# Optimization experiments

Measured on AMD Instinct MI355X. Metric: run time of the kernel, lower is better.

## Reference

```python
import jax, jax.numpy as jnp
import numpy as np

B, S, D = 4, 1024, 1024
DB = 128           # d_bottleneck (router embedding dim)
R = 128            # neuron bottleneck rank
N_QK, N_V, N_KNOW = 2048, 2048, 4096
MB_QK, MB_V, MB_KNOW = 16, 16, 32
H = 16
EPS = 1e-8


def _unit(k, shape):
    v = jax.random.normal(k, shape, jnp.float32)
    return v / (jnp.linalg.norm(v, axis=-1, keepdims=True) + EPS)


def setup_inputs() -> dict:
    key = jax.random.key(0)
    ks = jax.random.split(key, 16)
    s = 0.02
    nrm = lambda k, sh, sc=0.02: jax.random.normal(k, sh, jnp.float32) * sc
    return {
        "x": jax.random.normal(ks[0], (B, S, D), jnp.float32),
        "qk_emb": _unit(ks[1], (N_QK, DB)),
        "v_emb": _unit(ks[2], (N_V, DB)),
        "know_emb": _unit(ks[3], (N_KNOW, DB)),
        "qk_f": nrm(ks[4], (MB_QK, D, R)),
        "qk_r": nrm(ks[5], (MB_QK, R, D)),
        "v_f": nrm(ks[6], (MB_V, D, R)),
        "v_r": nrm(ks[7], (MB_V, R, D)),
        "know_f": nrm(ks[8], (MB_KNOW, D, R)),
        "know_r": nrm(ks[9], (MB_KNOW, R, D)),
        "proj_attn_k": nrm(ks[10], (D, 3 * DB)),
        "proj_attn_b": jnp.zeros((3 * DB,), jnp.float32),
        "tau_attn_k": nrm(ks[11], (D, 3)),
        "tau_attn_b": jnp.zeros((3,), jnp.float32),
        "proj_know_k": nrm(ks[12], (D, DB)),
        "proj_know_b": jnp.zeros((DB,), jnp.float32),
        "tau_know_k": nrm(ks[13], (D, 1)),
        "tau_know_b": jnp.zeros((1,), jnp.float32),
        "expand_O": nrm(ks[14], (D, D)),
        "ln1_scale": jnp.ones((D,), jnp.float32),
        "ln1_bias": jnp.zeros((D,), jnp.float32),
        "ln2_scale": jnp.ones((D,), jnp.float32),
        "ln2_bias": jnp.zeros((D,), jnp.float32),
    }


def layer_norm(x, scale, bias, eps=1e-6):
    mean = jnp.mean(x, axis=-1, keepdims=True)
    var = jnp.mean(jnp.square(x - mean), axis=-1, keepdims=True)
    return (x - mean) / jnp.sqrt(var + eps) * scale + bias


def threshold_gate(scores, tau):
    gate = jnp.maximum(scores - tau, 0.0)
    return gate / (gate.sum(axis=-1, keepdims=True) + EPS)


def group_gate(gate, n_basis):
    b, s, n = gate.shape  # n divisible by n_basis here
    g = gate.reshape(b, s, n_basis, n // n_basis).sum(axis=-1)
    return g / (g.sum(axis=-1, keepdims=True) + EPS)


@jax.checkpoint
def feature_fn(x, neurons, weights):
    all_h = jnp.einsum('bsd,ndr->bsnr', x, neurons)
    return jnp.einsum('bsnr,bsn->bsr', all_h, weights)


@jax.checkpoint
def restore_fn(h, neurons, weights):
    pre = jnp.einsum('bsr,bsn->bsnr', h, weights)
    return jnp.einsum('bsnr,nrd->bsd', pre, neurons)


def reference(x, qk_emb, v_emb, know_emb, qk_f, qk_r, v_f, v_r, know_f, know_r,
              proj_attn_k, proj_attn_b, tau_attn_k, tau_attn_b,
              proj_know_k, proj_know_b, tau_know_k, tau_know_b,
              expand_O, ln1_scale, ln1_bias, ln2_scale, ln2_bias):
    # ---- attention circuit (pre-LN) ----
    n1 = layer_norm(x, ln1_scale, ln1_bias)
    qk_n = qk_emb / (jnp.linalg.norm(qk_emb, axis=-1, keepdims=True) + EPS)
    v_n = v_emb / (jnp.linalg.norm(v_emb, axis=-1, keepdims=True) + EPS)
    h_all = n1 @ proj_attn_k + proj_attn_b            # [B,S,3*DB]
    h_q, h_k, h_v = jnp.split(h_all, 3, axis=-1)
    tau = n1 @ tau_attn_k + tau_attn_b                # [B,S,3]
    g_q = threshold_gate(h_q @ qk_n.T, tau[:, :, 0:1])
    g_k = threshold_gate(h_k @ qk_n.T, tau[:, :, 1:2])
    g_v = threshold_gate(h_v @ v_n.T, tau[:, :, 2:3])
    gq_b = group_gate(g_q, MB_QK)
    gk_b = group_gate(g_k, MB_QK)
    gv_b = group_gate(g_v, MB_V)
    Q = restore_fn(feature_fn(n1, qk_f, gq_b), qk_r, gq_b)
    K = restore_fn(feature_fn(n1, qk_f, gk_b), qk_r, gk_b)
    V = restore_fn(feature_fn(n1, v_f, gv_b), v_r, gv_b)
    d_head = D // H
    Q = Q.reshape(B, S, H, d_head).transpose(0, 2, 1, 3)
    K = K.reshape(B, S, H, d_head).transpose(0, 2, 1, 3)
    V = V.reshape(B, S, H, d_head).transpose(0, 2, 1, 3)
    scores = jnp.einsum('bhsd,bhtd->bhst', Q, K) / jnp.sqrt(jnp.float32(d_head))
    causal = jnp.tril(jnp.ones((S, S), dtype=jnp.bool_))
    scores = jnp.where(causal, scores, jnp.finfo(scores.dtype).min)
    attn_w = jax.nn.softmax(scores, axis=-1)
    attn_out = jnp.einsum('bhst,bhtd->bhsd', attn_w, V)
    attn_out = attn_out.transpose(0, 2, 1, 3).reshape(B, S, D) @ expand_O
    t_qk, t_v = 1.0 / N_QK, 1.0 / N_V
    a_aux = (((g_q.mean(axis=(0, 1)) - t_qk) ** 2).sum() * N_QK +
             ((g_k.mean(axis=(0, 1)) - t_qk) ** 2).sum() * N_QK +
             ((g_v.mean(axis=(0, 1)) - t_v) ** 2).sum() * N_V)
    x = x + attn_out
    # ---- knowledge circuit (pre-LN) ----
    n2 = layer_norm(x, ln2_scale, ln2_bias)
    know_n = know_emb / (jnp.linalg.norm(know_emb, axis=-1, keepdims=True) + EPS)
    h = n2 @ proj_know_k + proj_know_b
    tau_k = n2 @ tau_know_k + tau_know_b
    gate = threshold_gate(h @ know_n.T, tau_k)
    g_b = group_gate(gate, MB_KNOW)
    know_out = restore_fn(feature_fn(n2, know_f, g_b), know_r, g_b)
    k_aux = ((gate.mean(axis=(0, 1)) - 1.0 / N_KNOW) ** 2).sum() * N_KNOW
    x = x + know_out
    return x, a_aux + k_aux
```

## Files before the change

kernel.cpp:

```cpp
#include <hip/hip_runtime.h>
#include <math.h>

static constexpr int T = 4096;
static constexpr int D = 1024;

typedef __bf16 bf16_t;
typedef bf16_t bf16x8 __attribute__((ext_vector_type(8)));
typedef bf16_t bf16x4 __attribute__((ext_vector_type(4)));
typedef float f32x4 __attribute__((ext_vector_type(4)));

#define GLDS16(g, l)                                                        \
  __builtin_amdgcn_global_load_lds(                                         \
      (const __attribute__((address_space(1))) void*)(g),                   \
      (__attribute__((address_space(3))) void*)(l), 16, 0, 0)


__global__ void zero1_kernel(float* p) { *p = 0.f; }

__global__ __launch_bounds__(256) void ln_kernel(
    const float* __restrict__ x, const float* __restrict__ scale,
    const float* __restrict__ bias, float* __restrict__ out_f,
    bf16_t* __restrict__ out_b)
{
  int t = blockIdx.x;
  const float* xr = x + (size_t)t * D;
  float v[4];
  float s1 = 0.f, s2 = 0.f;
#pragma unroll
  for (int i = 0; i < 4; i++) {
    v[i] = xr[threadIdx.x + i * 256];
    s1 += v[i];
    s2 += v[i] * v[i];
  }
#pragma unroll
  for (int o = 1; o < 64; o <<= 1) {
    s1 += __shfl_xor(s1, o);
    s2 += __shfl_xor(s2, o);
  }
  __shared__ float r1[4], r2[4];
  int wid = threadIdx.x >> 6;
  if ((threadIdx.x & 63) == 0) { r1[wid] = s1; r2[wid] = s2; }
  __syncthreads();
  s1 = r1[0] + r1[1] + r1[2] + r1[3];
  s2 = r2[0] + r2[1] + r2[2] + r2[3];
  float mean = s1 * (1.f / D);
  float var = s2 * (1.f / D) - mean * mean;
  float rstd = rsqrtf(var + 1e-6f);
  float* orow = out_f + (size_t)t * D;
  bf16_t* brow = out_b + (size_t)t * D;
#pragma unroll
  for (int i = 0; i < 4; i++) {
    int d = threadIdx.x + i * 256;
    float o = (v[i] - mean) * rstd * scale[d] + bias[d];
    orow[d] = o;
    brow[d] = (bf16_t)o;
  }
}

__global__ __launch_bounds__(64) void norm_rows_kernel(
    const float* __restrict__ e, bf16_t* __restrict__ o)
{
  int r = blockIdx.x;
  const float* row = e + (size_t)r * 128;
  float a = row[threadIdx.x], b = row[threadIdx.x + 64];
  float ss = a * a + b * b;
#pragma unroll
  for (int m = 1; m < 64; m <<= 1) ss += __shfl_xor(ss, m);
  float inv = 1.f / (sqrtf(ss) + 1e-8f);
  bf16_t* orow = o + (size_t)r * 128;
  orow[threadIdx.x] = (bf16_t)(a * inv);
  orow[threadIdx.x + 64] = (bf16_t)(b * inv);
}

__global__ __launch_bounds__(64) void tau_kernel(
    const float* __restrict__ n, const float* __restrict__ W,
    const float* __restrict__ b, float* __restrict__ out, int J)
{
  int t = blockIdx.x;
  const float* nr = n + (size_t)t * D;
  for (int j = 0; j < J; j++) {
    float p = 0.f;
#pragma unroll 4
    for (int i = 0; i < 16; i++) {
      int d = threadIdx.x + i * 64;
      p += nr[d] * W[d * J + j];
    }
#pragma unroll
    for (int m = 1; m < 64; m <<= 1) p += __shfl_xor(p, m);
    if (threadIdx.x == 0) out[t * J + j] = p + b[j];
  }
}

template <int PER>
__global__ __launch_bounds__(256) void gate_kernel(
    float* __restrict__ g, const float* __restrict__ tau, int tauStride,
    int tauOff, float* __restrict__ gb, int N, int G)
{
  int t = blockIdx.x;
  float tv = tau[t * tauStride + tauOff];
  float* row = g + (size_t)t * N;
  float r[PER];
  int base = threadIdx.x * PER;
  float psum = 0.f;
#pragma unroll
  for (int i = 0; i < PER; i++) {
    float s = row[base + i] - tv;
    s = fmaxf(s, 0.f);
    r[i] = s;
    psum += s;
  }
  __shared__ float red[4];
  __shared__ float grp[32];
  if (threadIdx.x < 32) grp[threadIdx.x] = 0.f;
  float w = psum;
#pragma unroll
  for (int m = 1; m < 64; m <<= 1) w += __shfl_xor(w, m);
  int wid = threadIdx.x >> 6;
  if ((threadIdx.x & 63) == 0) red[wid] = w;
  __syncthreads();
  float Stot = red[0] + red[1] + red[2] + red[3];
  atomicAdd(&grp[base >> 7], psum);
  __syncthreads();
  float inv = 1.f / (Stot + 1e-8f);
#pragma unroll
  for (int i = 0; i < PER; i++) row[base + i] = r[i] * inv;
  if (threadIdx.x < G) {
    float Gj = grp[threadIdx.x] * inv;
    float gsum = Stot * inv;
    gb[(size_t)t * G + threadIdx.x] = Gj / (gsum + 1e-8f);
  }
}

__global__ __launch_bounds__(256) void colsum_part_kernel(
    const float* __restrict__ g, int N, float* __restrict__ colsum)
{
  int c = blockIdx.x * 256 + threadIdx.x;
  int r0 = blockIdx.y * 128;
  const float* p = g + (size_t)r0 * N + c;
  float s = 0.f;
#pragma unroll 8
  for (int t = 0; t < 128; t++) s += p[(size_t)t * N];
  atomicAdd(&colsum[c], s);
}

__global__ __launch_bounds__(256) void colsum_fin_kernel(
    const float* __restrict__ colsum, int N, float tinv,
    float* __restrict__ aux)
{
  int c = blockIdx.x * 256 + threadIdx.x;
  float mdev = colsum[c] * (1.f / T) - tinv;
  float p = mdev * mdev * (float)N;
#pragma unroll
  for (int m = 1; m < 64; m <<= 1) p += __shfl_xor(p, m);
  __shared__ float red[4];
  if ((threadIdx.x & 63) == 0) red[threadIdx.x >> 6] = p;
  __syncthreads();
  if (threadIdx.x == 0) atomicAdd(aux, red[0] + red[1] + red[2] + red[3]);
}

__global__ __launch_bounds__(128) void wsum2_kernel(
    const bf16_t* __restrict__ all_h, const float* __restrict__ gb1,
    const float* __restrict__ gb2, float* __restrict__ h1,
    float* __restrict__ h2, int NB)
{
  int t = blockIdx.x;
  int r = threadIdx.x;
  const bf16_t* row = all_h + (size_t)t * NB * 128;
  float a1 = 0.f, a2 = 0.f;
  for (int n = 0; n < NB; n++) {
    float v = (float)row[n * 128 + r];
    a1 += gb1[(size_t)t * NB + n] * v;
    if (gb2) a2 += gb2[(size_t)t * NB + n] * v;
  }
  h1[(size_t)t * 128 + r] = a1;
  if (h2) h2[(size_t)t * 128 + r] = a2;
}

__global__ __launch_bounds__(256) void transpose_to_bf16_kernel(
    const float* __restrict__ src, bf16_t* __restrict__ dst,
    int R, int C, size_t sbs, size_t dbs)
{
  __shared__ float tile[32][33];
  int b = blockIdx.z;
  int c0 = blockIdx.x * 32, r0 = blockIdx.y * 32;
  int tx = threadIdx.x & 31, ty = threadIdx.x >> 5;
  const float* s = src + (size_t)b * sbs;
  bf16_t* d = dst + (size_t)b * dbs;
#pragma unroll
  for (int i = 0; i < 4; i++)
    tile[ty + i * 8][tx] = s[(size_t)(r0 + ty + i * 8) * C + c0 + tx];
  __syncthreads();
#pragma unroll
  for (int i = 0; i < 4; i++)
    d[(size_t)(c0 + ty + i * 8) * R + r0 + tx] = (bf16_t)tile[tx][ty + i * 8];
}

__global__ __launch_bounds__(256) void avirt_kernel(
    const float* __restrict__ h, const float* __restrict__ gb, int NB,
    bf16_t* __restrict__ A, int K)
{
  int t = blockIdx.x;
  const float* hr = h + (size_t)t * 128;
  const float* gr = gb + (size_t)t * NB;
  bf16_t* ar = A + (size_t)t * K;
  int noct = K >> 3;
  for (int o = threadIdx.x; o < noct; o += 256) {
    int k = o * 8;
    float g = gr[k >> 7];
    bf16x8 v;
#pragma unroll
    for (int i = 0; i < 8; i++) v[i] = (bf16_t)(hr[(k & 127) + i] * g);
    *(bf16x8*)(ar + k) = v;
  }
}

__global__ __launch_bounds__(256) void combine2_kernel(
    const float* __restrict__ p0, const float* __restrict__ p1,
    float* __restrict__ out)
{
  int i = blockIdx.x * 256 + threadIdx.x;
  float4 a = ((const float4*)p0)[i];
  float4 b = ((const float4*)p1)[i];
  float4 o = ((float4*)out)[i];
  o.x += a.x + b.x;
  o.y += a.y + b.y;
  o.z += a.z + b.z;
  o.w += a.w + b.w;
  ((float4*)out)[i] = o;
}

template <bool HAS_BIAS, bool HAS_RESID, int OUT_MODE>
__global__ __launch_bounds__(256) void mfma_gemm_kernel(
    const bf16_t* __restrict__ A, int lda,
    const bf16_t* __restrict__ Bt, int ldb,
    void* __restrict__ Cv, int ldc,
    const float* __restrict__ bias,
    const float* __restrict__ resid, int ldr,
    int M, int N, int K)
{
  __shared__ bf16_t As[2][64 * 32];
  __shared__ bf16_t Bs[2][128 * 32];
  int tid = threadIdx.x;
  int wave = tid >> 6, lane = tid & 63;

  unsigned lid = blockIdx.y * gridDim.x + blockIdx.x;
  unsigned nwg = gridDim.x * gridDim.y;
  unsigned swzb = lid;
  if ((nwg & 7u) == 0u) swzb = (lid & 7u) * (nwg >> 3) + (lid >> 3);
  int row0 = (int)(swzb / gridDim.x) * 64;
  int col0 = (int)(swzb % gridDim.x) * 128;

  int wr = (wave >> 1) * 32, wc = (wave & 1) * 64;

  f32x4 acc[2][4] = {};

  int srow = (wave << 4) + (lane >> 2);
  int g8 = (((lane & 3) ^ ((srow >> 1) & 3)) << 3);
  const bf16_t* gA = A + (size_t)(row0 + srow) * lda + g8;
  const bf16_t* gB = Bt + (size_t)(col0 + srow) * ldb + g8;
  size_t b64 = (size_t)64 * ldb;

  int fr = lane & 15, fq = lane >> 4;

#define GSTAGE(buf, k0s)                                  \
  {                                                       \
    GLDS16(gA + (k0s), &As[buf][wave * 512]);             \
    GLDS16(gB + (k0s), &Bs[buf][wave * 512]);             \
    GLDS16(gB + b64 + (k0s), &Bs[buf][2048 + wave * 512]);\
  }

  GSTAGE(0, 0);
  int cur = 0;
  for (int k0 = 0; k0 < K; k0 += 32) {
    __syncthreads();
    if (k0 + 32 < K) GSTAGE(cur ^ 1, k0 + 32);
    bf16x8 af[2], bfr[4];
#pragma unroll
    for (int m = 0; m < 2; m++) {
      int R = wr + m * 16 + fr;
      af[m] = *(const bf16x8*)&As[cur][R * 32 + ((fq ^ ((R >> 1) & 3)) << 3)];
    }
#pragma unroll
    for (int n = 0; n < 4; n++) {
      int R = wc + n * 16 + fr;
      bfr[n] = *(const bf16x8*)&Bs[cur][R * 32 + ((fq ^ ((R >> 1) & 3)) << 3)];
    }
#pragma unroll
    for (int m = 0; m < 2; m++)
#pragma unroll
      for (int n = 0; n < 4; n++)
        acc[m][n] = __builtin_amdgcn_mfma_f32_16x16x32_bf16(af[m], bfr[n],
                                                            acc[m][n], 0, 0, 0);
    cur ^= 1;
  }
#undef GSTAGE

#pragma unroll
  for (int m = 0; m < 2; m++) {
#pragma unroll
    for (int n = 0; n < 4; n++) {
      int rowb = row0 + wr + m * 16 + fq * 4;
      int col = col0 + wc + n * 16 + fr;
      if (OUT_MODE == 2) {
        bf16x4 v4;
#pragma unroll
        for (int r = 0; r < 4; r++) v4[r] = (bf16_t)acc[m][n][r];
        bf16_t* dst = (bf16_t*)Cv +
            ((size_t)(rowb >> 10) * 1024 + col) * 1024 + (rowb & 1023);
        *(bf16x4*)dst = v4;
      } else {
#pragma unroll
        for (int r = 0; r < 4; r++) {
          int row = rowb + r;
          float v = acc[m][n][r];
          if (HAS_BIAS) v += bias[col];
          if (HAS_RESID) v += resid[(size_t)row * ldr + col];
          if (OUT_MODE == 1)
            ((bf16_t*)Cv)[(size_t)row * ldc + col] = (bf16_t)v;
          else
            ((float*)Cv)[(size_t)row * ldc + col] = v;
        }
      }
    }
  }
}

struct ZArg { const bf16_t* A; const bf16_t* Bt; void* C; int mode; };

__global__ __launch_bounds__(256) void mfma_gemm_batched_kernel(
    ZArg za, ZArg zb, ZArg zc, int lda, int ldb, int ldc, int K)
{
  __shared__ bf16_t As[2][64 * 32];
  __shared__ bf16_t Bs[2][128 * 32];
  int tid = threadIdx.x;
  int wave = tid >> 6, lane = tid & 63;

  unsigned gx = gridDim.x;
  unsigned gxy = gridDim.x * gridDim.y;
  unsigned lid = (blockIdx.z * gridDim.y + blockIdx.y) * gx + blockIdx.x;
  unsigned nwg = gxy * gridDim.z;
  unsigned swzb = lid;
  if ((nwg & 7u) == 0u) swzb = (lid & 7u) * (nwg >> 3) + (lid >> 3);
  unsigned zi = swzb / gxy;
  unsigned rem = swzb % gxy;
  int row0 = (int)(rem / gx) * 64;
  int col0 = (int)(rem % gx) * 128;
  ZArg Z = (zi == 0) ? za : (zi == 1) ? zb : zc;

  int wr = (wave >> 1) * 32, wc = (wave & 1) * 64;
  f32x4 acc[2][4] = {};

  int srow = (wave << 4) + (lane >> 2);
  int g8 = (((lane & 3) ^ ((srow >> 1) & 3)) << 3);
  const bf16_t* gA = Z.A + (size_t)(row0 + srow) * lda + g8;
  const bf16_t* gB = Z.Bt + (size_t)(col0 + srow) * ldb + g8;
  size_t b64 = (size_t)64 * ldb;

  int fr = lane & 15, fq = lane >> 4;

#define GSTAGE(buf, k0s)                                  \
  {                                                       \
    GLDS16(gA + (k0s), &As[buf][wave * 512]);             \
    GLDS16(gB + (k0s), &Bs[buf][wave * 512]);             \
    GLDS16(gB + b64 + (k0s), &Bs[buf][2048 + wave * 512]);\
  }

  GSTAGE(0, 0);
  int cur = 0;
  for (int k0 = 0; k0 < K; k0 += 32) {
    __syncthreads();
    if (k0 + 32 < K) GSTAGE(cur ^ 1, k0 + 32);
    bf16x8 af[2], bfr[4];
#pragma unroll
    for (int m = 0; m < 2; m++) {
      int R = wr + m * 16 + fr;
      af[m] = *(const bf16x8*)&As[cur][R * 32 + ((fq ^ ((R >> 1) & 3)) << 3)];
    }
#pragma unroll
    for (int n = 0; n < 4; n++) {
      int R = wc + n * 16 + fr;
      bfr[n] = *(const bf16x8*)&Bs[cur][R * 32 + ((fq ^ ((R >> 1) & 3)) << 3)];
    }
#pragma unroll
    for (int m = 0; m < 2; m++)
#pragma unroll
      for (int n = 0; n < 4; n++)
        acc[m][n] = __builtin_amdgcn_mfma_f32_16x16x32_bf16(af[m], bfr[n],
                                                            acc[m][n], 0, 0, 0);
    cur ^= 1;
  }
#undef GSTAGE

#pragma unroll
  for (int m = 0; m < 2; m++) {
#pragma unroll
    for (int n = 0; n < 4; n++) {
      int rowb = row0 + wr + m * 16 + fq * 4;
      int col = col0 + wc + n * 16 + fr;
      if (Z.mode == 2) {
        bf16x4 v4;
#pragma unroll
        for (int r = 0; r < 4; r++) v4[r] = (bf16_t)acc[m][n][r];
        bf16_t* dst = (bf16_t*)Z.C +
            ((size_t)(rowb >> 10) * 1024 + col) * 1024 + (rowb & 1023);
        *(bf16x4*)dst = v4;
      } else if (Z.mode == 1) {
#pragma unroll
        for (int r = 0; r < 4; r++)
          ((bf16_t*)Z.C)[(size_t)(rowb + r) * ldc + col] =
              (bf16_t)acc[m][n][r];
      } else {
#pragma unroll
        for (int r = 0; r < 4; r++)
          ((float*)Z.C)[(size_t)(rowb + r) * ldc + col] = acc[m][n][r];
      }
    }
  }
}

__global__ __launch_bounds__(512) void flash_mfma_kernel(
    const bf16_t* __restrict__ Q, const bf16_t* __restrict__ K,
    const bf16_t* __restrict__ Vt, bf16_t* __restrict__ O)
{
  __shared__ bf16_t Ks[2][64 * 64];
  __shared__ bf16_t Vs[2][64 * 64];
  __shared__ bf16_t Pl[8][32 * 64];

  int tid = threadIdx.x;
  int wave = tid >> 6, lane = tid & 63;
  int fr = lane & 15, fq = lane >> 4;
  unsigned lid = blockIdx.x + blockIdx.y * 4 + blockIdx.z * 64;
  unsigned swz8 = (lid & 7u) * 32 + (lid >> 3);
  int s_slot = swz8 & 3;
  unsigned hb = swz8 >> 2;
  int h = hb & 15, b = hb >> 4;
  int half = wave >> 2, w4 = wave & 3;
  int qb = half ? (7 - s_slot) : s_slot;
  int q0w = qb * 128 + w4 * 32;
  int KT = 16 - 2 * s_slot;
  size_t qkbase = ((size_t)b * 1024) * 1024 + (size_t)h * 64;
  size_t vtbase = ((size_t)b * 1024 + (size_t)h * 64) * 1024;

  int srow8 = lane >> 3;
  int scb = (((lane & 7) << 4) ^ (srow8 << 4)) >> 1;

#define FSTAGE(buf, kt)                                                     \
  {                                                                         \
    int k0s = (kt) * 64;                                                    \
    int row = wave * 8 + srow8;                                             \
    GLDS16(&K[qkbase + (size_t)(k0s + row) * 1024 + scb],                   \
           &Ks[buf][wave * 512]);                                           \
    GLDS16(&Vt[vtbase + (size_t)row * 1024 + k0s + scb],                    \
           &Vs[buf][wave * 512]);                                           \
  }

  bf16x8 qf[2][2];
#pragma unroll
  for (int g = 0; g < 2; g++)
#pragma unroll
    for (int kh = 0; kh < 2; kh++)
      qf[g][kh] = *(const bf16x8*)&Q[qkbase +
                                     (size_t)(q0w + g * 16 + fr) * 1024 +
                                     kh * 32 + fq * 8];

  f32x4 o_acc[2][4] = {};
  float mrow[2][4], lrow[2][4];
#pragma unroll
  for (int g = 0; g < 2; g++)
#pragma unroll
    for (int r = 0; r < 4; r++) { mrow[g][r] = -INFINITY; lrow[g][r] = 0.f; }

  char* P = (char*)&Pl[wave][0];

  FSTAGE(0, 0);

  for (int kt = 0; kt < KT; kt++) {
    __syncthreads();
    if (kt + 1 < KT) FSTAGE((kt + 1) & 1, kt + 1);
    int k0 = kt * 64;
    if (k0 <= q0w + 31) {
      const char* Kb = (const char*)&Ks[kt & 1][0];
      const char* Vb = (const char*)&Vs[kt & 1][0];
      int swz = (fr & 7) << 4;
      f32x4 s[2][4] = {};
#pragma unroll
      for (int n = 0; n < 4; n++) {
        int rowo = (n * 16 + fr) * 128;
        bf16x8 kf0 = *(const bf16x8*)(Kb + rowo + ((fq * 16) ^ swz));
        bf16x8 kf1 = *(const bf16x8*)(Kb + rowo + ((64 + fq * 16) ^ swz));
#pragma unroll
        for (int g = 0; g < 2; g++) {
          s[g][n] = __builtin_amdgcn_mfma_f32_16x16x32_bf16(qf[g][0], kf0,
                                                            s[g][n], 0, 0, 0);
          s[g][n] = __builtin_amdgcn_mfma_f32_16x16x32_bf16(qf[g][1], kf1,
                                                            s[g][n], 0, 0, 0);
        }
      }
      const float scale = 0.125f;
#pragma unroll
      for (int g = 0; g < 2; g++) {
        bool dm = (k0 + 63 > q0w + g * 16);
#pragma unroll
        for (int n = 0; n < 4; n++)
#pragma unroll
          for (int r = 0; r < 4; r++) {
            float v = s[g][n][r] * scale;
            if (dm && (k0 + n * 16 + fr > q0w + g * 16 + fq * 4 + r))
              v = -INFINITY;
            s[g][n][r] = v;
          }
      }
      float corr[2][4];
#pragma unroll
      for (int g = 0; g < 2; g++)
#pragma unroll
        for (int r = 0; r < 4; r++) {
          float mx = fmaxf(fmaxf(s[g][0][r], s[g][1][r]),
                           fmaxf(s[g][2][r], s[g][3][r]));
#pragma unroll
          for (int msk = 1; msk < 16; msk <<= 1)
            mx = fmaxf(mx, __shfl_xor(mx, msk));
          float mnew = fmaxf(mrow[g][r], mx);
          corr[g][r] = __expf(mrow[g][r] - mnew);
          mrow[g][r] = mnew;
          float ps = 0.f;
#pragma unroll
          for (int n = 0; n < 4; n++) {
            float p = __expf(s[g][n][r] - mnew);
            s[g][n][r] = p;
            ps += p;
          }
#pragma unroll
          for (int msk = 1; msk < 16; msk <<= 1) ps += __shfl_xor(ps, msk);
          lrow[g][r] = lrow[g][r] * corr[g][r] + ps;
        }
#pragma unroll
      for (int g = 0; g < 2; g++)
#pragma unroll
        for (int n = 0; n < 4; n++)
#pragma unroll
          for (int r = 0; r < 4; r++) {
            int q = g * 16 + fq * 4 + r;
            int cb = ((n * 16 + fr) * 2) ^ ((q & 7) << 4);
            *(bf16_t*)(P + q * 128 + cb) = (bf16_t)s[g][n][r];
          }
      int rr = fr & 3;
      int srcl = (fr >> 2) << 4;
#pragma unroll
      for (int g = 0; g < 2; g++) {
        float c0 = __shfl(corr[g][0], srcl);
        float c1 = __shfl(corr[g][1], srcl);
        float c2 = __shfl(corr[g][2], srcl);
        float c3 = __shfl(corr[g][3], srcl);
        float cq = rr == 0 ? c0 : rr == 1 ? c1 : rr == 2 ? c2 : c3;
#pragma unroll
        for (int n = 0; n < 4; n++)
#pragma unroll
          for (int r = 0; r < 4; r++) o_acc[g][n][r] *= cq;
      }
#pragma unroll
      for (int c = 0; c < 2; c++) {
        bf16x8 pf[2];
#pragma unroll
        for (int g = 0; g < 2; g++)
          pf[g] = *(const bf16x8*)(P + (g * 16 + fr) * 128 +
                                   ((c * 64 + fq * 16) ^ swz));
#pragma unroll
        for (int n = 0; n < 4; n++) {
          bf16x8 vf = *(const bf16x8*)(Vb + (n * 16 + fr) * 128 +
                                       ((c * 64 + fq * 16) ^ swz));
#pragma unroll
          for (int g = 0; g < 2; g++)
            o_acc[g][n] = __builtin_amdgcn_mfma_f32_16x16x32_bf16(
                vf, pf[g], o_acc[g][n], 0, 0, 0);
        }
      }
    }
  }
  int rr = fr & 3;
  int srcl = (fr >> 2) << 4;
#pragma unroll
  for (int g = 0; g < 2; g++) {
    float l0 = __shfl(lrow[g][0], srcl);
    float l1 = __shfl(lrow[g][1], srcl);
    float l2 = __shfl(lrow[g][2], srcl);
    float l3 = __shfl(lrow[g][3], srcl);
    float lq = rr == 0 ? l0 : rr == 1 ? l1 : rr == 2 ? l2 : l3;
    float linv = 1.f / lq;
    size_t orow = qkbase + (size_t)(q0w + g * 16 + fr) * 1024;
#pragma unroll
    for (int n = 0; n < 4; n++) {
      bf16x4 ov;
#pragma unroll
      for (int r = 0; r < 4; r++) ov[r] = (bf16_t)(o_acc[g][n][r] * linv);
      *(bf16x4*)&O[orow + n * 16 + fq * 4] = ov;
    }
  }
#undef FSTAGE
}


extern "C" void kernel_launch(void* const* d_in, const int* in_sizes, int n_in,
                              void* d_out, int out_size, void* d_ws,
                              size_t ws_size, hipStream_t stream) {
  (void)in_sizes; (void)n_in; (void)out_size; (void)ws_size;
  const float* x          = (const float*)d_in[0];
  const float* qk_emb     = (const float*)d_in[1];
  const float* v_emb      = (const float*)d_in[2];
  const float* know_emb   = (const float*)d_in[3];
  const float* qk_f       = (const float*)d_in[4];
  const float* qk_r       = (const float*)d_in[5];
  const float* v_f        = (const float*)d_in[6];
  const float* v_r        = (const float*)d_in[7];
  const float* know_f     = (const float*)d_in[8];
  const float* know_r     = (const float*)d_in[9];
  const float* proj_attn_k = (const float*)d_in[10];
  const float* proj_attn_b = (const float*)d_in[11];
  const float* tau_attn_k  = (const float*)d_in[12];
  const float* tau_attn_b  = (const float*)d_in[13];
  const float* proj_know_k = (const float*)d_in[14];
  const float* proj_know_b = (const float*)d_in[15];
  const float* tau_know_k  = (const float*)d_in[16];
  const float* tau_know_b  = (const float*)d_in[17];
  const float* expand_O    = (const float*)d_in[18];
  const float* ln1_scale   = (const float*)d_in[19];
  const float* ln1_bias    = (const float*)d_in[20];
  const float* ln2_scale   = (const float*)d_in[21];
  const float* ln2_bias    = (const float*)d_in[22];

  float* out = (float*)d_out;
  float* aux = out + (size_t)T * D;

  float* ws = (float*)d_ws;
  float* n_f   = ws;
  float* tau3  = n_f + 4194304;
  float* gq_b  = tau3 + 16384;
  float* gk_b  = gq_b + 65536;
  float* gv_b  = gk_b + 65536;
  float* gkn_b = gv_b + 65536;
  float* csum  = gkn_b + 131072;
  float* hQ    = csum + 4096;
  float* hK    = hQ + 524288;
  float* hV    = hK + 524288;
  float* qkvarena = hV + 524288;
  float* buf_big = qkvarena + 12582912;

  bf16_t* Qbb = (bf16_t*)qkvarena;
  bf16_t* Kbb = Qbb + (size_t)T * 1024;
  bf16_t* Vtb = Kbb + (size_t)T * 1024;

  bf16_t* nb   = (bf16_t*)(buf_big + 16777216);
  bf16_t* hab  = nb + 4194304;
  bf16_t* embB = hab + 1572864;
  bf16_t* B2t  = embB + 524288;
  bf16_t* wt   = B2t + 4194304;
  bf16_t* pa_t  = wt;
  bf16_t* qkr_t = pa_t + 393216;
  bf16_t* vr_t  = qkr_t + 2097152;
  bf16_t* knr_t = vr_t + 2097152;
  bf16_t* eo_t  = knr_t + 4194304;
  bf16_t* pk_t  = eo_t + 1048576;

  bf16_t* avbQ = (bf16_t*)buf_big;
  bf16_t* avbK = avbQ + (size_t)T * 2048;
  bf16_t* avbV = avbK + (size_t)T * 2048;
  bf16_t* avbN = (bf16_t*)buf_big;
  float* kp0 = buf_big + 8388608;
  float* kp1 = kp0 + 4194304;
  bf16_t* allh_b = (bf16_t*)buf_big;
  bf16_t* attnb_b = (bf16_t*)(buf_big + 12582912);

  bf16_t* embQ = embB;
  bf16_t* embV = embB + 262144;

  dim3 blk(256);

  zero1_kernel<<<1, 1, 0, stream>>>(aux);

  transpose_to_bf16_kernel<<<dim3(12, 32, 1), blk, 0, stream>>>(
      proj_attn_k, pa_t, 1024, 384, 0, 0);
  transpose_to_bf16_kernel<<<dim3(32, 64, 1), blk, 0, stream>>>(
      qk_r, qkr_t, 2048, 1024, 0, 0);
  transpose_to_bf16_kernel<<<dim3(32, 64, 1), blk, 0, stream>>>(
      v_r, vr_t, 2048, 1024, 0, 0);
  transpose_to_bf16_kernel<<<dim3(32, 128, 1), blk, 0, stream>>>(
      know_r, knr_t, 4096, 1024, 0, 0);
  transpose_to_bf16_kernel<<<dim3(32, 32, 1), blk, 0, stream>>>(
      expand_O, eo_t, 1024, 1024, 0, 0);
  transpose_to_bf16_kernel<<<dim3(4, 32, 1), blk, 0, stream>>>(
      proj_know_k, pk_t, 1024, 128, 0, 0);

  ln_kernel<<<T, blk, 0, stream>>>(x, ln1_scale, ln1_bias, n_f, nb);
  norm_rows_kernel<<<2048, 64, 0, stream>>>(qk_emb, embQ);
  norm_rows_kernel<<<2048, 64, 0, stream>>>(v_emb, embV);

  mfma_gemm_kernel<true, false, 1><<<dim3(3, 64), blk, 0, stream>>>(
      nb, 1024, pa_t, 1024, hab, 384, proj_attn_b, nullptr, 0, T, 384, 1024);
  tau_kernel<<<T, 64, 0, stream>>>(n_f, tau_attn_k, tau_attn_b, tau3, 3);

  mfma_gemm_kernel<false, false, 0><<<dim3(16, 64), blk, 0, stream>>>(
      hab + 0, 384, embQ, 128, buf_big, 2048, nullptr, nullptr, 0, T, 2048, 128);
  gate_kernel<8><<<T, blk, 0, stream>>>(buf_big, tau3, 3, 0, gq_b, 2048, 16);
  hipMemsetAsync(csum, 0, 2048 * sizeof(float), stream);
  colsum_part_kernel<<<dim3(8, 32), blk, 0, stream>>>(buf_big, 2048, csum);
  colsum_fin_kernel<<<8, blk, 0, stream>>>(csum, 2048, 1.f / 2048.f, aux);

  mfma_gemm_kernel<false, false, 0><<<dim3(16, 64), blk, 0, stream>>>(
      hab + 128, 384, embQ, 128, buf_big, 2048, nullptr, nullptr, 0, T, 2048, 128);
  gate_kernel<8><<<T, blk, 0, stream>>>(buf_big, tau3, 3, 1, gk_b, 2048, 16);
  hipMemsetAsync(csum, 0, 2048 * sizeof(float), stream);
  colsum_part_kernel<<<dim3(8, 32), blk, 0, stream>>>(buf_big, 2048, csum);
  colsum_fin_kernel<<<8, blk, 0, stream>>>(csum, 2048, 1.f / 2048.f, aux);

  mfma_gemm_kernel<false, false, 0><<<dim3(16, 64), blk, 0, stream>>>(
      hab + 256, 384, embV, 128, buf_big, 2048, nullptr, nullptr, 0, T, 2048, 128);
  gate_kernel<8><<<T, blk, 0, stream>>>(buf_big, tau3, 3, 2, gv_b, 2048, 16);
  hipMemsetAsync(csum, 0, 2048 * sizeof(float), stream);
  colsum_part_kernel<<<dim3(8, 32), blk, 0, stream>>>(buf_big, 2048, csum);
  colsum_fin_kernel<<<8, blk, 0, stream>>>(csum, 2048, 1.f / 2048.f, aux);

  transpose_to_bf16_kernel<<<dim3(4, 32, 16), blk, 0, stream>>>(
      qk_f, B2t, 1024, 128, 131072, 131072);
  mfma_gemm_kernel<false, false, 1><<<dim3(16, 64), blk, 0, stream>>>(
      nb, 1024, B2t, 1024, allh_b, 2048, nullptr, nullptr, 0, T, 2048, 1024);
  wsum2_kernel<<<T, 128, 0, stream>>>(allh_b, gq_b, gk_b, hQ, hK, 16);

  transpose_to_bf16_kernel<<<dim3(4, 32, 16), blk, 0, stream>>>(
      v_f, B2t, 1024, 128, 131072, 131072);
  mfma_gemm_kernel<false, false, 1><<<dim3(16, 64), blk, 0, stream>>>(
      nb, 1024, B2t, 1024, allh_b, 2048, nullptr, nullptr, 0, T, 2048, 1024);
  wsum2_kernel<<<T, 128, 0, stream>>>(allh_b, gv_b, nullptr, hV, nullptr, 16);

  avirt_kernel<<<T, blk, 0, stream>>>(hQ, gq_b, 16, avbQ, 2048);
  avirt_kernel<<<T, blk, 0, stream>>>(hK, gk_b, 16, avbK, 2048);
  avirt_kernel<<<T, blk, 0, stream>>>(hV, gv_b, 16, avbV, 2048);
  {
    ZArg zq{avbQ, qkr_t, Qbb, 1};
    ZArg zk{avbK, qkr_t, Kbb, 1};
    ZArg zv{avbV, vr_t, Vtb, 2};
    mfma_gemm_batched_kernel<<<dim3(8, 64, 3), blk, 0, stream>>>(
        zq, zk, zv, 2048, 2048, 1024, 2048);
  }

  flash_mfma_kernel<<<dim3(4, 16, 4), dim3(512), 0, stream>>>(Qbb, Kbb, Vtb,
                                                              attnb_b);
  mfma_gemm_kernel<false, true, 0><<<dim3(8, 64), blk, 0, stream>>>(
      attnb_b, 1024, eo_t, 1024, out, 1024, nullptr, x, 1024, T, 1024, 1024);

  ln_kernel<<<T, blk, 0, stream>>>(out, ln2_scale, ln2_bias, n_f, nb);
  norm_rows_kernel<<<4096, 64, 0, stream>>>(know_emb, embB);
  mfma_gemm_kernel<true, false, 1><<<dim3(1, 64), blk, 0, stream>>>(
      nb, 1024, pk_t, 1024, hab, 128, proj_know_b, nullptr, 0, T, 128, 1024);
  tau_kernel<<<T, 64, 0, stream>>>(n_f, tau_know_k, tau_know_b, tau3, 1);

  mfma_gemm_kernel<false, false, 0><<<dim3(32, 64), blk, 0, stream>>>(
      hab, 128, embB, 128, buf_big, 4096, nullptr, nullptr, 0, T, 4096, 128);
  gate_kernel<16><<<T, blk, 0, stream>>>(buf_big, tau3, 1, 0, gkn_b, 4096, 32);
  hipMemsetAsync(csum, 0, 4096 * sizeof(float), stream);
  colsum_part_kernel<<<dim3(16, 32), blk, 0, stream>>>(buf_big, 4096, csum);
  colsum_fin_kernel<<<16, blk, 0, stream>>>(csum, 4096, 1.f / 4096.f, aux);

  transpose_to_bf16_kernel<<<dim3(4, 32, 32), blk, 0, stream>>>(
      know_f, B2t, 1024, 128, 131072, 131072);
  mfma_gemm_kernel<false, false, 1><<<dim3(32, 64), blk, 0, stream>>>(
      nb, 1024, B2t, 1024, allh_b, 4096, nullptr, nullptr, 0, T, 4096, 1024);
  wsum2_kernel<<<T, 128, 0, stream>>>(allh_b, gkn_b, nullptr, hQ, nullptr, 32);

  avirt_kernel<<<T, blk, 0, stream>>>(hQ, gkn_b, 32, avbN, 4096);
  {
    ZArg z0{avbN, knr_t, kp0, 0};
    ZArg z1{avbN + 2048, knr_t + 2048, kp1, 0};
    mfma_gemm_batched_kernel<<<dim3(8, 64, 2), blk, 0, stream>>>(
        z0, z1, z0, 4096, 4096, 1024, 2048);
  }
  combine2_kernel<<<4096, blk, 0, stream>>>(kp0, kp1, out);
}
```

Measured before the change: 672.0 us.

## Batch Q/K/V routing GEMMs, gating, colsum, feature GEMMs into grid-z launches

```diff
diff --git a/kernel.cpp b/kernel.cpp
--- a/kernel.cpp
+++ b/kernel.cpp
@@ -92,13 +92,9 @@
 }
 
 template <int PER>
-__global__ __launch_bounds__(256) void gate_kernel(
-    float* __restrict__ g, const float* __restrict__ tau, int tauStride,
-    int tauOff, float* __restrict__ gb, int N, int G)
-{
-  int t = blockIdx.x;
-  float tv = tau[t * tauStride + tauOff];
-  float* row = g + (size_t)t * N;
+__device__ __forceinline__ void gate_body(
+    float* __restrict__ row, float tv, float* __restrict__ gb, int G)
+{
   float r[PER];
   int base = threadIdx.x * PER;
   float psum = 0.f;
@@ -127,8 +123,30 @@
   if (threadIdx.x < G) {
     float Gj = grp[threadIdx.x] * inv;
     float gsum = Stot * inv;
-    gb[(size_t)t * G + threadIdx.x] = Gj / (gsum + 1e-8f);
-  }
+    gb[threadIdx.x] = Gj / (gsum + 1e-8f);
+  }
+}
+
+template <int PER>
+__global__ __launch_bounds__(256) void gate_kernel(
+    float* __restrict__ g, const float* __restrict__ tau, int tauStride,
+    int tauOff, float* __restrict__ gb, int N, int G)
+{
+  int t = blockIdx.x;
+  gate_body<PER>(g + (size_t)t * N, tau[t * tauStride + tauOff],
+                 gb + (size_t)t * G, G);
+}
+
+template <int PER>
+__global__ __launch_bounds__(256) void gate3_kernel(
+    float* __restrict__ s0, float* __restrict__ s1, float* __restrict__ s2,
+    const float* __restrict__ tau, float* __restrict__ g0,
+    float* __restrict__ g1, float* __restrict__ g2, int N, int G)
+{
+  int t = blockIdx.x, y = blockIdx.y;
+  float* g = y == 0 ? s0 : y == 1 ? s1 : s2;
+  float* gb = y == 0 ? g0 : y == 1 ? g1 : g2;
+  gate_body<PER>(g + (size_t)t * N, tau[t * 3 + y], gb + (size_t)t * G, G);
 }
 
 __global__ __launch_bounds__(256) void colsum_part_kernel(
@@ -141,6 +159,21 @@
 #pragma unroll 8
   for (int t = 0; t < 128; t++) s += p[(size_t)t * N];
   atomicAdd(&colsum[c], s);
+}
+
+__global__ __launch_bounds__(256) void colsum_part3_kernel(
+    const float* __restrict__ s0, const float* __restrict__ s1,
+    const float* __restrict__ s2, int N, float* __restrict__ colsum)
+{
+  int z = blockIdx.z;
+  const float* g = z == 0 ? s0 : z == 1 ? s1 : s2;
+  int c = blockIdx.x * 256 + threadIdx.x;
+  int r0 = blockIdx.y * 128;
+  const float* p = g + (size_t)r0 * N + c;
+  float s = 0.f;
+#pragma unroll 8
+  for (int t = 0; t < 128; t++) s += p[(size_t)t * N];
+  atomicAdd(&colsum[z * N + c], s);
 }
 
 __global__ __launch_bounds__(256) void colsum_fin_kernel(
@@ -176,6 +209,31 @@
   if (h2) h2[(size_t)t * 128 + r] = a2;
 }
 
+__global__ __launch_bounds__(128) void wsum2b_kernel(
+    const bf16_t* __restrict__ aq, const bf16_t* __restrict__ av,
+    const float* __restrict__ gq, const float* __restrict__ gk,
+    const float* __restrict__ gv, float* __restrict__ hQ,
+    float* __restrict__ hK, float* __restrict__ hV, int NB)
+{
+  int t = blockIdx.x, y = blockIdx.y;
+  int r = threadIdx.x;
+  const bf16_t* row = (y == 0 ? aq : av) + (size_t)t * NB * 128;
+  const float* g1 = (y == 0 ? gq : gv) + (size_t)t * NB;
+  const float* g2 = y == 0 ? gk + (size_t)t * NB : nullptr;
+  float a1 = 0.f, a2 = 0.f;
+  for (int n = 0; n < NB; n++) {
+    float v = (float)row[n * 128 + r];
+    a1 += g1[n] * v;
+    if (g2) a2 += g2[n] * v;
+  }
+  if (y == 0) {
+    hQ[(size_t)t * 128 + r] = a1;
+    hK[(size_t)t * 128 + r] = a2;
+  } else {
+    hV[(size_t)t * 128 + r] = a1;
+  }
+}
+
 __global__ __launch_bounds__(256) void transpose_to_bf16_kernel(
     const float* __restrict__ src, bf16_t* __restrict__ dst,
     int R, int C, size_t sbs, size_t dbs)
@@ -195,14 +253,9 @@
     d[(size_t)(c0 + ty + i * 8) * R + r0 + tx] = (bf16_t)tile[tx][ty + i * 8];
 }
 
-__global__ __launch_bounds__(256) void avirt_kernel(
-    const float* __restrict__ h, const float* __restrict__ gb, int NB,
-    bf16_t* __restrict__ A, int K)
-{
-  int t = blockIdx.x;
-  const float* hr = h + (size_t)t * 128;
-  const float* gr = gb + (size_t)t * NB;
-  bf16_t* ar = A + (size_t)t * K;
+__device__ __forceinline__ void avirt_body(
+    const float* hr, const float* gr, bf16_t* ar, int K)
+{
   int noct = K >> 3;
   for (int o = threadIdx.x; o < noct; o += 256) {
     int k = o * 8;
@@ -212,6 +265,28 @@
     for (int i = 0; i < 8; i++) v[i] = (bf16_t)(hr[(k & 127) + i] * g);
     *(bf16x8*)(ar + k) = v;
   }
+}
+
+__global__ __launch_bounds__(256) void avirt_kernel(
+    const float* __restrict__ h, const float* __restrict__ gb, int NB,
+    bf16_t* __restrict__ A, int K)
+{
+  int t = blockIdx.x;
+  avirt_body(h + (size_t)t * 128, gb + (size_t)t * NB, A + (size_t)t * K, K);
+}
+
+__global__ __launch_bounds__(256) void avirt3_kernel(
+    const float* __restrict__ h0, const float* __restrict__ h1,
+    const float* __restrict__ h2, const float* __restrict__ g0,
+    const float* __restrict__ g1, const float* __restrict__ g2, int NB,
+    bf16_t* __restrict__ A0, bf16_t* __restrict__ A1,
+    bf16_t* __restrict__ A2, int K)
+{
+  int t = blockIdx.x, y = blockIdx.y;
+  const float* h = y == 0 ? h0 : y == 1 ? h1 : h2;
+  const float* g = y == 0 ? g0 : y == 1 ? g1 : g2;
+  bf16_t* A = y == 0 ? A0 : y == 1 ? A1 : A2;
+  avirt_body(h + (size_t)t * 128, g + (size_t)t * NB, A + (size_t)t * K, K);
 }
 
 __global__ __launch_bounds__(256) void combine2_kernel(
@@ -251,7 +326,6 @@
   int col0 = (int)(swzb % gridDim.x) * 128;
 
   int wr = (wave >> 1) * 32, wc = (wave & 1) * 64;
-
   f32x4 acc[2][4] = {};
 
   int srow = (wave << 4) + (lane >> 2);
@@ -639,7 +713,7 @@
   float* gv_b  = gk_b + 65536;
   float* gkn_b = gv_b + 65536;
   float* csum  = gkn_b + 131072;
-  float* hQ    = csum + 4096;
+  float* hQ    = csum + 8192;
   float* hK    = hQ + 524288;
   float* hV    = hK + 524288;
   float* qkvarena = hV + 524288;
@@ -660,14 +734,20 @@
   bf16_t* knr_t = vr_t + 2097152;
   bf16_t* eo_t  = knr_t + 4194304;
   bf16_t* pk_t  = eo_t + 1048576;
-
+  bf16_t* B2t2  = pk_t + 131072;
+
+  float* s_q = buf_big;
+  float* s_k = buf_big + 8388608;
+  float* s_v = (float*)qkvarena;
+  bf16_t* allh_q = (bf16_t*)buf_big;
+  bf16_t* allh_v = allh_q + (size_t)T * 2048;
   bf16_t* avbQ = (bf16_t*)buf_big;
   bf16_t* avbK = avbQ + (size_t)T * 2048;
   bf16_t* avbV = avbK + (size_t)T * 2048;
   bf16_t* avbN = (bf16_t*)buf_big;
+  bf16_t* allh_n = (bf16_t*)buf_big;
   float* kp0 = buf_big + 8388608;
   float* kp1 = kp0 + 4194304;
-  bf16_t* allh_b = (bf16_t*)buf_big;
   bf16_t* attnb_b = (bf16_t*)(buf_big + 12582912);
 
   bf16_t* embQ = embB;
@@ -689,6 +769,10 @@
       expand_O, eo_t, 1024, 1024, 0, 0);
   transpose_to_bf16_kernel<<<dim3(4, 32, 1), blk, 0, stream>>>(
       proj_know_k, pk_t, 1024, 128, 0, 0);
+  transpose_to_bf16_kernel<<<dim3(4, 32, 16), blk, 0, stream>>>(
+      qk_f, B2t, 1024, 128, 131072, 131072);
+  transpose_to_bf16_kernel<<<dim3(4, 32, 16), blk, 0, stream>>>(
+      v_f, B2t2, 1024, 128, 131072, 131072);
 
   ln_kernel<<<T, blk, 0, stream>>>(x, ln1_scale, ln1_bias, n_f, nb);
   norm_rows_kernel<<<2048, 64, 0, stream>>>(qk_emb, embQ);
@@ -698,42 +782,31 @@
       nb, 1024, pa_t, 1024, hab, 384, proj_attn_b, nullptr, 0, T, 384, 1024);
   tau_kernel<<<T, 64, 0, stream>>>(n_f, tau_attn_k, tau_attn_b, tau3, 3);
 
-  mfma_gemm_kernel<false, false, 0><<<dim3(16, 64), blk, 0, stream>>>(
-      hab + 0, 384, embQ, 128, buf_big, 2048, nullptr, nullptr, 0, T, 2048, 128);
-  gate_kernel<8><<<T, blk, 0, stream>>>(buf_big, tau3, 3, 0, gq_b, 2048, 16);
-  hipMemsetAsync(csum, 0, 2048 * sizeof(float), stream);
-  colsum_part_kernel<<<dim3(8, 32), blk, 0, stream>>>(buf_big, 2048, csum);
-  colsum_fin_kernel<<<8, blk, 0, stream>>>(csum, 2048, 1.f / 2048.f, aux);
-
-  mfma_gemm_kernel<false, false, 0><<<dim3(16, 64), blk, 0, stream>>>(
-      hab + 128, 384, embQ, 128, buf_big, 2048, nullptr, nullptr, 0, T, 2048, 128);
-  gate_kernel<8><<<T, blk, 0, stream>>>(buf_big, tau3, 3, 1, gk_b, 2048, 16);
-  hipMemsetAsync(csum, 0, 2048 * sizeof(float), stream);
-  colsum_part_kernel<<<dim3(8, 32), blk, 0, stream>>>(buf_big, 2048, csum);
-  colsum_fin_kernel<<<8, blk, 0, stream>>>(csum, 2048, 1.f / 2048.f, aux);
-
-  mfma_gemm_kernel<false, false, 0><<<dim3(16, 64), blk, 0, stream>>>(
-      hab + 256, 384, embV, 128, buf_big, 2048, nullptr, nullptr, 0, T, 2048, 128);
-  gate_kernel<8><<<T, blk, 0, stream>>>(buf_big, tau3, 3, 2, gv_b, 2048, 16);
-  hipMemsetAsync(csum, 0, 2048 * sizeof(float), stream);
-  colsum_part_kernel<<<dim3(8, 32), blk, 0, stream>>>(buf_big, 2048, csum);
-  colsum_fin_kernel<<<8, blk, 0, stream>>>(csum, 2048, 1.f / 2048.f, aux);
-
-  transpose_to_bf16_kernel<<<dim3(4, 32, 16), blk, 0, stream>>>(
-      qk_f, B2t, 1024, 128, 131072, 131072);
-  mfma_gemm_kernel<false, false, 1><<<dim3(16, 64), blk, 0, stream>>>(
-      nb, 1024, B2t, 1024, allh_b, 2048, nullptr, nullptr, 0, T, 2048, 1024);
-  wsum2_kernel<<<T, 128, 0, stream>>>(allh_b, gq_b, gk_b, hQ, hK, 16);
-
-  transpose_to_bf16_kernel<<<dim3(4, 32, 16), blk, 0, stream>>>(
-      v_f, B2t, 1024, 128, 131072, 131072);
-  mfma_gemm_kernel<false, false, 1><<<dim3(16, 64), blk, 0, stream>>>(
-      nb, 1024, B2t, 1024, allh_b, 2048, nullptr, nullptr, 0, T, 2048, 1024);
-  wsum2_kernel<<<T, 128, 0, stream>>>(allh_b, gv_b, nullptr, hV, nullptr, 16);
-
-  avirt_kernel<<<T, blk, 0, stream>>>(hQ, gq_b, 16, avbQ, 2048);
-  avirt_kernel<<<T, blk, 0, stream>>>(hK, gk_b, 16, avbK, 2048);
-  avirt_kernel<<<T, blk, 0, stream>>>(hV, gv_b, 16, avbV, 2048);
+  {
+    ZArg zq{hab + 0, embQ, s_q, 0};
+    ZArg zk{hab + 128, embQ, s_k, 0};
+    ZArg zv{hab + 256, embV, s_v, 0};
+    mfma_gemm_batched_kernel<<<dim3(16, 64, 3), blk, 0, stream>>>(
+        zq, zk, zv, 384, 128, 2048, 128);
+  }
+  gate3_kernel<8><<<dim3(T, 3), blk, 0, stream>>>(
+      s_q, s_k, s_v, tau3, gq_b, gk_b, gv_b, 2048, 16);
+  hipMemsetAsync(csum, 0, 6144 * sizeof(float), stream);
+  colsum_part3_kernel<<<dim3(8, 32, 3), blk, 0, stream>>>(s_q, s_k, s_v,
+                                                          2048, csum);
+  colsum_fin_kernel<<<24, blk, 0, stream>>>(csum, 2048, 1.f / 2048.f, aux);
+
+  {
+    ZArg zf1{nb, B2t, allh_q, 1};
+    ZArg zf2{nb, B2t2, allh_v, 1};
+    mfma_gemm_batched_kernel<<<dim3(16, 64, 2), blk, 0, stream>>>(
+        zf1, zf2, zf1, 1024, 1024, 2048, 1024);
+  }
+  wsum2b_kernel<<<dim3(T, 2), 128, 0, stream>>>(allh_q, allh_v, gq_b, gk_b,
+                                                gv_b, hQ, hK, hV, 16);
+
+  avirt3_kernel<<<dim3(T, 3), blk, 0, stream>>>(hQ, hK, hV, gq_b, gk_b, gv_b,
+                                                16, avbQ, avbK, avbV, 2048);
   {
     ZArg zq{avbQ, qkr_t, Qbb, 1};
     ZArg zk{avbK, qkr_t, Kbb, 1};
@@ -763,8 +836,8 @@
   transpose_to_bf16_kernel<<<dim3(4, 32, 32), blk, 0, stream>>>(
       know_f, B2t, 1024, 128, 131072, 131072);
   mfma_gemm_kernel<false, false, 1><<<dim3(32, 64), blk, 0, stream>>>(
-      nb, 1024, B2t, 1024, allh_b, 4096, nullptr, nullptr, 0, T, 4096, 1024);
-  wsum2_kernel<<<T, 128, 0, stream>>>(allh_b, gkn_b, nullptr, hQ, nullptr, 32);
+      nb, 1024, B2t, 1024, allh_n, 4096, nullptr, nullptr, 0, T, 4096, 1024);
+  wsum2_kernel<<<T, 128, 0, stream>>>(allh_n, gkn_b, nullptr, hQ, nullptr, 32);
 
   avirt_kernel<<<T, blk, 0, stream>>>(hQ, gkn_b, 32, avbN, 4096);
   {
```

Measured after the change: 628.2 us. -6.5%, faster.
